# Performance work log

Measured on AMD Instinct MI355X. Metric: run time of the kernel, lower is better.

The kernel has to match this reference:

```python
import jax, jax.numpy as jnp
import numpy as np

WS = 7   # window_size
SS = 3   # shift_size = window_size // 2
NH = 16  # num_heads


def _rel_pos_index(ws):
    coords = np.stack(np.meshgrid(np.arange(ws), np.arange(ws), indexing='ij'))  # (2, ws, ws)
    cf = coords.reshape(2, -1)
    rel = (cf[:, :, None] - cf[:, None, :]).transpose(1, 2, 0)
    rel[:, :, 0] += ws - 1
    rel[:, :, 1] += ws - 1
    rel[:, :, 0] *= 2 * ws - 1
    return rel.sum(-1)  # (ws*ws, ws*ws) int

REL_IDX = _rel_pos_index(WS)


def _attn_mask(h, w, ws, ss):
    img = np.zeros((h, w))
    sls = (slice(0, -ws), slice(-ws, -ss), slice(-ss, None))
    cnt = 0
    for i in sls:
        for j in sls:
            img[i, j] = cnt
            cnt += 1
    mw = img.reshape(h // ws, ws, w // ws, ws).transpose(0, 2, 1, 3).reshape(-1, ws * ws)
    d = mw[:, None, :] - mw[:, :, None]  # (nW, N, N)
    return np.where(d != 0, -100.0, 0.0).astype(np.float32)


def _part(x, ws):
    b, h, w, c = x.shape
    return x.reshape(b, h // ws, ws, w // ws, ws, c).transpose(0, 1, 3, 2, 4, 5).reshape(-1, ws * ws, c)


def _rev(win, ws, h, w):
    c = win.shape[-1]
    b = win.shape[0] // ((h // ws) * (w // ws))
    return win.reshape(b, h // ws, w // ws, ws, ws, c).transpose(0, 1, 3, 2, 4, 5).reshape(b, h, w, c)


def _ln(x, g, b):
    m = x.mean(-1, keepdims=True)
    v = x.var(-1, keepdims=True)
    return (x - m) / jnp.sqrt(v + 1e-5) * g + b


def _wattn(x, qkv_w, qkv_b, proj_w, proj_b, table, mask):
    B_, N, C = x.shape
    hd = C // NH
    scale = hd ** -0.5
    qkv = (x @ qkv_w.T + qkv_b).reshape(B_, N, 3, NH, hd).transpose(2, 0, 3, 1, 4)
    q, k, v = qkv[0] * scale, qkv[1], qkv[2]  # (B_, NH, N, hd)
    attn = jnp.einsum('bhnd,bhmd->bhnm', q, k)
    bias = table[REL_IDX.reshape(-1)].reshape(N, N, NH).transpose(2, 0, 1)  # (NH, N, N)
    attn = attn + bias[None]
    if mask is not None:
        nW = mask.shape[0]
        attn = (attn.reshape(B_ // nW, nW, NH, N, N) + mask[None, :, None]).reshape(B_, NH, N, N)
    attn = jax.nn.softmax(attn, axis=-1)
    out = jnp.einsum('bhnm,bhmd->bhnd', attn, v).transpose(0, 2, 1, 3).reshape(B_, N, C)
    return out @ proj_w.T + proj_b


def _mlp(x, w1, b1, w2, b2):
    return jax.nn.gelu(x @ w1.T + b1, approximate=False) @ w2.T + b2


def _forward(x, w_norm1_g, w_norm1_b, w_qkv_w, w_qkv_b, w_proj_w, w_proj_b, w_table,
             w_norm2_g, w_norm2_b, w_fc1_w, w_fc1_b, w_fc2_w, w_fc2_b,
             sw_norm1_g, sw_norm1_b, sw_qkv_w, sw_qkv_b, sw_proj_w, sw_proj_b, sw_table,
             sw_norm2_g, sw_norm2_b, sw_fc1_w, sw_fc1_b, sw_fc2_w, sw_fc2_b):
    b, c, h, w = x.shape
    x = jnp.transpose(x, (0, 2, 3, 1)).reshape(b, h * w, c)  # (B, HW, C)
    shortcut = x
    xn = _ln(x, w_norm1_g, w_norm1_b).reshape(b, h, w, c)
    aw = _wattn(_part(xn, WS), w_qkv_w, w_qkv_b, w_proj_w, w_proj_b, w_table, None)
    x = shortcut + _rev(aw, WS, h, w).reshape(b, h * w, c)
    x = x + _mlp(_ln(x, w_norm2_g, w_norm2_b), w_fc1_w, w_fc1_b, w_fc2_w, w_fc2_b)
    # shifted-window branch (shift_size > 0 since min(h,w) > window_size)
    xn = _ln(x, sw_norm1_g, sw_norm1_b)
    mask = jnp.asarray(_attn_mask(h, w, WS, SS))
    shifted = jnp.roll(xn.reshape(b, h, w, c), (-SS, -SS), axis=(1, 2))
    sa = _wattn(_part(shifted, WS), sw_qkv_w, sw_qkv_b, sw_proj_w, sw_proj_b, sw_table, mask)
    shifted = jnp.roll(_rev(sa, WS, h, w), (SS, SS), axis=(1, 2)).reshape(b, h * w, c)
    # NOTE: source adds the residual to the *normalized* activations here; kept faithful.
    x = xn + shifted
    x = x + _mlp(_ln(x, sw_norm2_g, sw_norm2_b), sw_fc1_w, sw_fc1_b, sw_fc2_w, sw_fc2_b)
    return x.reshape(b, h, w, c)


def setup_inputs() -> dict:
    key = jax.random.key(0)
    ks = jax.random.split(key, 32)
    B, C, H, W = 8, 512, 56, 56
    Cm = 4 * C
    T = (2 * WS - 1) ** 2

    def rn(k, shape, s=0.02):
        return jax.random.normal(k, shape, jnp.float32) * s

    d = {'x': jax.random.normal(ks[0], (B, C, H, W), jnp.float32)}
    for i, p in enumerate(['w', 'sw']):
        o = 1 + i * 6
        d[p + '_norm1_g'] = jnp.ones((C,), jnp.float32)
        d[p + '_norm1_b'] = jnp.zeros((C,), jnp.float32)
        d[p + '_qkv_w'] = rn(ks[o], (3 * C, C))
        d[p + '_qkv_b'] = jnp.zeros((3 * C,), jnp.float32)
        d[p + '_proj_w'] = rn(ks[o + 1], (C, C))
        d[p + '_proj_b'] = jnp.zeros((C,), jnp.float32)
        d[p + '_table'] = rn(ks[o + 2], (T, NH))
        d[p + '_norm2_g'] = jnp.ones((C,), jnp.float32)
        d[p + '_norm2_b'] = jnp.zeros((C,), jnp.float32)
        d[p + '_fc1_w'] = rn(ks[o + 3], (Cm, C))
        d[p + '_fc1_b'] = jnp.zeros((Cm,), jnp.float32)
        d[p + '_fc2_w'] = rn(ks[o + 4], (C, Cm))
        d[p + '_fc2_b'] = jnp.zeros((C,), jnp.float32)
    return d


def reference(x, w_norm1_g, w_norm1_b, w_qkv_w, w_qkv_b, w_proj_w, w_proj_b, w_table,
              w_norm2_g, w_norm2_b, w_fc1_w, w_fc1_b, w_fc2_w, w_fc2_b,
              sw_norm1_g, sw_norm1_b, sw_qkv_w, sw_qkv_b, sw_proj_w, sw_proj_b, sw_table,
              sw_norm2_g, sw_norm2_b, sw_fc1_w, sw_fc1_b, sw_fc2_w, sw_fc2_b):
    return _forward(x, w_norm1_g, w_norm1_b, w_qkv_w, w_qkv_b, w_proj_w, w_proj_b, w_table,
                    w_norm2_g, w_norm2_b, w_fc1_w, w_fc1_b, w_fc2_w, w_fc2_b,
                    sw_norm1_g, sw_norm1_b, sw_qkv_w, sw_qkv_b, sw_proj_w, sw_proj_b, sw_table,
                    sw_norm2_g, sw_norm2_b, sw_fc1_w, sw_fc1_b, sw_fc2_w, sw_fc2_b)
```

## Files before the change

kernel.cpp:

```cpp
#include <hip/hip_runtime.h>
#include <hip/hip_bf16.h>

using bf16 = __hip_bfloat16;

#define B_      8
#define C_      512
#define H_      56
#define W_      56
#define HW_     3136
#define M_      25088
#define NH_     16
#define HD_     32
#define WS_     7
#define NT_     49

typedef __attribute__((ext_vector_type(8))) short bf16x8;
typedef __attribute__((ext_vector_type(4))) float f32x4;

#define AS1(p) ((const __attribute__((address_space(1))) void*)(p))
#define AS3(p) ((__attribute__((address_space(3))) void*)(p))

__device__ inline float bf2f(const bf16 v) {
    unsigned short u = *reinterpret_cast<const unsigned short*>(&v);
    return __uint_as_float((unsigned)u << 16);
}
__device__ inline unsigned short f2bfu(float f) {
    bf16 h = __float2bfloat16(f);
    return *reinterpret_cast<unsigned short*>(&h);
}
__device__ inline float rdv(const float* p) { return *p; }
__device__ inline float rdv(const bf16* p)  { return bf2f(*p); }
__device__ inline void stv(float* p, float v) { *p = v; }
__device__ inline void stv(bf16* p, float v)  { *p = __float2bfloat16(v); }

__device__ inline float gelu_t(float v) {
    const float u = v * (0.79788456080286536f + 0.035677408136300125f * v * v);
    const float e = __expf(2.0f * u);
    return 0.5f * v * (2.0f - 2.0f / (e + 1.0f));
}

__global__ void k_detect(const void* g1, int* flag) {
    const unsigned short* u = (const unsigned short*)g1;
    *flag = (u[0] == 0x3F80u) ? 1 : 0;
}

struct WArgs {
    const void* src[26];
    bf16*       dst[26];
    int         n[26];
};
__global__ __launch_bounds__(256) void k_convert_all(WArgs a, const int* flag) {
    const int isb = *flag;
    const int gid = blockIdx.x * 256 + threadIdx.x;
    const int stride = gridDim.x * 256;
    #pragma unroll 1
    for (int w = 0; w < 26; ++w) {
        const int n = a.n[w];
        bf16* d = a.dst[w];
        if (isb) {
            const unsigned short* s = (const unsigned short*)a.src[w];
            for (int i = gid; i < n; i += stride) ((unsigned short*)d)[i] = s[i];
        } else {
            const float* s = (const float*)a.src[w];
            for (int i = gid; i < n; i += stride) d[i] = __float2bfloat16(s[i]);
        }
    }
}

__global__ __launch_bounds__(256) void k_transpose_in(const void* xin, bf16* X,
                                                      const int* flag) {
    __shared__ float tile[32][33];
    const int isb = *flag;
    const int p0 = blockIdx.x * 32, c0 = blockIdx.y * 32, b = blockIdx.z;
    const int tp = threadIdx.x & 31, tc = threadIdx.x >> 5;
    const size_t ibase = (size_t)b * C_ * HW_;
    #pragma unroll
    for (int i = 0; i < 4; ++i) {
        const int c = tc + i * 8;
        const size_t idx = ibase + (size_t)(c0 + c) * HW_ + p0 + tp;
        tile[c][tp] = isb ? bf2f(((const bf16*)xin)[idx]) : ((const float*)xin)[idx];
    }
    __syncthreads();
    const int wc = threadIdx.x & 31, wp = threadIdx.x >> 5;
    bf16* dst = X + (size_t)b * HW_ * C_;
    #pragma unroll
    for (int i = 0; i < 4; ++i) {
        const int p = wp + i * 8;
        dst[(size_t)(p0 + p) * C_ + c0 + wc] = __float2bfloat16(tile[wc][p]);
    }
}

__global__ __launch_bounds__(128) void k_layernorm(const bf16* __restrict__ X,
                                                   const bf16* __restrict__ g,
                                                   const bf16* __restrict__ bta,
                                                   bf16* __restrict__ XN) {
    const int tok = blockIdx.x;
    const ushort4 u = reinterpret_cast<const ushort4*>(X + (size_t)tok * C_)[threadIdx.x];
    float4 v;
    v.x = __uint_as_float((unsigned)u.x << 16);
    v.y = __uint_as_float((unsigned)u.y << 16);
    v.z = __uint_as_float((unsigned)u.z << 16);
    v.w = __uint_as_float((unsigned)u.w << 16);
    float s  = v.x + v.y + v.z + v.w;
    float s2 = v.x * v.x + v.y * v.y + v.z * v.z + v.w * v.w;
    #pragma unroll
    for (int o = 32; o > 0; o >>= 1) { s += __shfl_down(s, o); s2 += __shfl_down(s2, o); }
    __shared__ float sh[4];
    if ((threadIdx.x & 63) == 0) { sh[threadIdx.x >> 6] = s; sh[2 + (threadIdx.x >> 6)] = s2; }
    __syncthreads();
    const float ts = sh[0] + sh[1], ts2 = sh[2] + sh[3];
    const float m = ts * (1.0f / C_);
    const float var = ts2 * (1.0f / C_) - m * m;
    const float r = rsqrtf(var + 1e-5f);
    const int c = threadIdx.x * 4;
    ushort4 o;
    o.x = f2bfu((v.x - m) * r * bf2f(g[c + 0]) + bf2f(bta[c + 0]));
    o.y = f2bfu((v.y - m) * r * bf2f(g[c + 1]) + bf2f(bta[c + 1]));
    o.z = f2bfu((v.z - m) * r * bf2f(g[c + 2]) + bf2f(bta[c + 2]));
    o.w = f2bfu((v.w - m) * r * bf2f(g[c + 3]) + bf2f(bta[c + 3]));
    reinterpret_cast<ushort4*>(XN + (size_t)tok * C_)[threadIdx.x] = o;
}

template <typename TADD, typename TO, bool GELU, bool ADD, bool FINAL>
__global__ __launch_bounds__(512, 2) void k_gemm8(const bf16* __restrict__ A,
                                                  const bf16* __restrict__ Wt,
                                                  const bf16* __restrict__ bias,
                                                  const TADD* __restrict__ addp,
                                                  TO* __restrict__ out,
                                                  const int* flag,
                                                  int N, int K) {
    __shared__ bf16 sA[2][2][128 * 64];
    __shared__ bf16 sB[2][2][128 * 64];
    const int tid  = threadIdx.x;
    const int lane = tid & 63;
    const int wid  = tid >> 6;
    const int wr   = wid >> 2;
    const int wc2  = wid & 3;
    const int bh   = wc2 >> 1;
    const int brl  = (wc2 & 1) * 64;

    const int nwg  = gridDim.x;
    const int orig = blockIdx.x;
    const int nx = nwg >> 3, rr_ = nwg & 7;
    const int xcd = orig & 7, offw = orig >> 3;
    const int wg = (xcd < rr_ ? xcd * (nx + 1) : rr_ * (nx + 1) + (xcd - rr_) * nx) + offw;
    const int gx = N >> 8;
    const int m0 = (wg / gx) * 256, n0 = (wg % gx) * 256;

    const f32x4 vz = {0.f, 0.f, 0.f, 0.f};
    f32x4 acc[8][4];
    #pragma unroll
    for (int i = 0; i < 8; ++i)
        #pragma unroll
        for (int j = 0; j < 4; ++j) acc[i][j] = vz;

    const int sr8  = lane >> 3;
    const int schk = (lane & 7) ^ sr8;
    const bf16* gA0 = A  + (size_t)(m0 + sr8) * K + schk * 8;
    const bf16* gB0 = Wt + (size_t)(n0 + sr8) * K + schk * 8;

    const int l15 = lane & 15, g4 = lane >> 4;
    const int NTL = K >> 6;
    const int NITER = NTL >> 1;

    auto stageA = [&](int d, int h, int T) {
        const int kt = T << 6;
        #pragma unroll
        for (int p = 0; p < 2; ++p) {
            const int q = wid * 2 + p;
            __builtin_amdgcn_global_load_lds(
                AS1(gA0 + (size_t)(h * 128 + q * 8) * K + kt),
                AS3(&sA[d][h][q * 512]), 16, 0, 0);
        }
    };
    auto stageB = [&](int d, int h, int T) {
        const int kt = T << 6;
        #pragma unroll
        for (int p = 0; p < 2; ++p) {
            const int q = wid * 2 + p;
            __builtin_amdgcn_global_load_lds(
                AS1(gB0 + (size_t)(h * 128 + q * 8) * K + kt),
                AS3(&sB[d][h][q * 512]), 16, 0, 0);
        }
    };

    stageA(0, 0, 0); stageA(0, 1, 0);
    stageB(0, 0, 0); stageB(0, 1, 0);
    stageB(1, 0, 1); stageB(1, 1, 1);
    asm volatile("s_waitcnt vmcnt(4)" ::: "memory");
    __builtin_amdgcn_s_barrier();

    #pragma unroll 1
    for (int it = 0; it < NITER; ++it) {
        const bool nl = (it < NITER - 1);
        #pragma unroll
        for (int half = 0; half < 2; ++half) {
            bf16x8 bfr[4][2];
            #pragma unroll
            for (int q = 0; q < 4; ++q) {
                if (q == 0) {
                    #pragma unroll
                    for (int ks = 0; ks < 2; ++ks) {
                        const int ch = ((ks << 2) | g4) ^ (l15 & 7);
                        #pragma unroll
                        for (int j = 0; j < 4; ++j) {
                            const int r = brl + j * 16 + l15;
                            bfr[j][ks] = *reinterpret_cast<const bf16x8*>(&sB[half][bh][r * 64 + ch * 8]);
                        }
                    }
                }
                bf16x8 af[2][2];
                #pragma unroll
                for (int ks = 0; ks < 2; ++ks) {
                    const int ch = ((ks << 2) | g4) ^ (l15 & 7);
                    #pragma unroll
                    for (int ii = 0; ii < 2; ++ii) {
                        const int r = (q * 2 + ii) * 16 + l15;
                        af[ii][ks] = *reinterpret_cast<const bf16x8*>(&sA[half][wr][r * 64 + ch * 8]);
                    }
                }
                if (half == 0) {
                    if (q == 0)            { stageA(1, 0, 2 * it + 1); stageA(1, 1, 2 * it + 1); }
                    else if (q == 1 && nl) { stageB(0, 0, 2 * it + 2); }
                    else if (q == 2 && nl) { stageB(0, 1, 2 * it + 2); }
                } else {
                    if (q == 0 && nl)      { stageA(0, 0, 2 * it + 2); }
                    else if (q == 1 && nl) { stageA(0, 1, 2 * it + 2); }
                    else if (q == 2 && nl) { stageB(1, 0, 2 * it + 3); }
                    else if (q == 3 && nl) { stageB(1, 1, 2 * it + 3); }
                }
                __builtin_amdgcn_s_barrier();
                asm volatile("s_waitcnt lgkmcnt(0)" ::: "memory");
                __builtin_amdgcn_s_setprio(1);
                #pragma unroll
                for (int ks = 0; ks < 2; ++ks)
                    #pragma unroll
                    for (int ii = 0; ii < 2; ++ii)
                        #pragma unroll
                        for (int j = 0; j < 4; ++j)
                            acc[q * 2 + ii][j] = __builtin_amdgcn_mfma_f32_16x16x32_bf16(
                                af[ii][ks], bfr[j][ks], acc[q * 2 + ii][j], 0, 0, 0);
                __builtin_amdgcn_s_setprio(0);
                if (q == 3) {
                    if (half == 0) {
                        if (nl) asm volatile("s_waitcnt vmcnt(4)" ::: "memory");
                        else    asm volatile("s_waitcnt vmcnt(0)" ::: "memory");
                    } else if (nl) {
                        asm volatile("s_waitcnt vmcnt(4)" ::: "memory");
                    }
                }
                __builtin_amdgcn_s_barrier();
            }
        }
    }

    int obf = 0;
    if constexpr (FINAL) obf = *flag;
    const int colBase = n0 + wc2 * 64 + l15;
    const int rowTop  = m0 + wr * 128 + g4 * 4;
    float bc[4];
    #pragma unroll
    for (int j = 0; j < 4; ++j) bc[j] = bf2f(bias[colBase + j * 16]);
    #pragma unroll
    for (int i = 0; i < 8; ++i) {
        #pragma unroll
        for (int r = 0; r < 4; ++r) {
            const int row = rowTop + i * 16 + r;
            #pragma unroll
            for (int j = 0; j < 4; ++j) {
                const int col = colBase + j * 16;
                float v = acc[i][j][r] + bc[j];
                if constexpr (GELU) v = gelu_t(v);
                if constexpr (ADD)  v += rdv(&addp[(size_t)row * N + col]);
                if constexpr (FINAL) {
                    if (obf) ((bf16*)(void*)out)[(size_t)row * N + col] = __float2bfloat16(v);
                    else     ((float*)(void*)out)[(size_t)row * N + col] = v;
                } else {
                    stv(&out[(size_t)row * N + col], v);
                }
            }
        }
    }
}

template <typename TADD, typename TO, bool GELU, bool ADD, bool FINAL>
__global__ __launch_bounds__(512, 2) void k_gemm_mfma(const bf16* __restrict__ A,
                                                      const bf16* __restrict__ Wt,
                                                      const bf16* __restrict__ bias,
                                                      const TADD* __restrict__ addp,
                                                      TO* __restrict__ out,
                                                      const int* flag,
                                                      int N, int K) {
    __shared__ bf16 sA[3][256 * 64];
    __shared__ bf16 sB[3][128 * 64];
    const int tid  = threadIdx.x;
    const int lane = tid & 63;
    const int wid  = tid >> 6;
    const int wr   = wid >> 1;
    const int wc2  = wid & 1;

    const int nwg  = gridDim.x;
    const int orig = blockIdx.x;
    const int nx = nwg >> 3, rr_ = nwg & 7;
    const int xcd = orig & 7, offw = orig >> 3;
    const int wg = (xcd < rr_ ? xcd * (nx + 1) : rr_ * (nx + 1) + (xcd - rr_) * nx) + offw;
    const int gx = N >> 7;
    const int m0 = (wg / gx) * 256, n0 = (wg % gx) * 128;

    const f32x4 vz = {0.f, 0.f, 0.f, 0.f};
    f32x4 acc[4][4];
    #pragma unroll
    for (int i = 0; i < 4; ++i)
        #pragma unroll
        for (int j = 0; j < 4; ++j) acc[i][j] = vz;

    const int sr8  = lane >> 3;
    const int schk = (lane & 7) ^ sr8;
    const bf16* gA0 = A  + (size_t)(m0 + sr8) * K + schk * 8;
    const bf16* gB0 = Wt + (size_t)(n0 + sr8) * K + schk * 8;

    const int l15 = lane & 15, g4 = lane >> 4;
    const int NTLE = K >> 6;

    #pragma unroll
    for (int tt = 0; tt < 3; ++tt) {
        const int kt = tt << 6;
        #pragma unroll
        for (int p = 0; p < 4; ++p) {
            const int q = wid * 4 + p;
            __builtin_amdgcn_global_load_lds(AS1(gA0 + (size_t)(q * 8) * K + kt),
                                             AS3(&sA[tt][q * 512]), 16, 0, 0);
        }
        #pragma unroll
        for (int p = 0; p < 2; ++p) {
            const int q = wid * 2 + p;
            __builtin_amdgcn_global_load_lds(AS1(gB0 + (size_t)(q * 8) * K + kt),
                                             AS3(&sB[tt][q * 512]), 16, 0, 0);
        }
    }

    for (int t = 0; t < NTLE; ++t) {
        const int rem = NTLE - 1 - t;
        if (rem >= 2)      asm volatile("s_waitcnt vmcnt(12)" ::: "memory");
        else if (rem == 1) asm volatile("s_waitcnt vmcnt(6)"  ::: "memory");
        else               asm volatile("s_waitcnt vmcnt(0)"  ::: "memory");
        __builtin_amdgcn_s_barrier();

        const int buf = t % 3;
        bf16x8 bfr[4][2];
        #pragma unroll
        for (int ks = 0; ks < 2; ++ks) {
            const int ch = ((ks << 2) | g4) ^ (l15 & 7);
            #pragma unroll
            for (int j = 0; j < 4; ++j) {
                const int rowB = wc2 * 64 + j * 16 + l15;
                bfr[j][ks] = *reinterpret_cast<const bf16x8*>(&sB[buf][rowB * 64 + ch * 8]);
            }
        }
        const int ch0 = g4 ^ (l15 & 7);
        const int ch1 = (4 | g4) ^ (l15 & 7);
        __builtin_amdgcn_s_setprio(1);
        #pragma unroll
        for (int i = 0; i < 4; ++i) {
            const int rowA = wr * 64 + i * 16 + l15;
            const bf16x8 a0 = *reinterpret_cast<const bf16x8*>(&sA[buf][rowA * 64 + ch0 * 8]);
            const bf16x8 a1 = *reinterpret_cast<const bf16x8*>(&sA[buf][rowA * 64 + ch1 * 8]);
            #pragma unroll
            for (int j = 0; j < 4; ++j) {
                acc[i][j] = __builtin_amdgcn_mfma_f32_16x16x32_bf16(a0, bfr[j][0], acc[i][j], 0, 0, 0);
                acc[i][j] = __builtin_amdgcn_mfma_f32_16x16x32_bf16(a1, bfr[j][1], acc[i][j], 0, 0, 0);
            }
        }
        __builtin_amdgcn_s_setprio(0);

        asm volatile("s_waitcnt lgkmcnt(0)" ::: "memory");
        __builtin_amdgcn_s_barrier();

        const int tn = t + 3;
        if (tn < NTLE) {
            const int kt = tn << 6;
            #pragma unroll
            for (int p = 0; p < 4; ++p) {
                const int q = wid * 4 + p;
                __builtin_amdgcn_global_load_lds(AS1(gA0 + (size_t)(q * 8) * K + kt),
                                                 AS3(&sA[buf][q * 512]), 16, 0, 0);
            }
            #pragma unroll
            for (int p = 0; p < 2; ++p) {
                const int q = wid * 2 + p;
                __builtin_amdgcn_global_load_lds(AS1(gB0 + (size_t)(q * 8) * K + kt),
                                                 AS3(&sB[buf][q * 512]), 16, 0, 0);
            }
        }
    }

    int obf = 0;
    if constexpr (FINAL) obf = *flag;
    const int colBase = n0 + wc2 * 64 + l15;
    const int rowTop  = m0 + wr * 64 + g4 * 4;
    float bc[4];
    #pragma unroll
    for (int j = 0; j < 4; ++j) bc[j] = bf2f(bias[colBase + j * 16]);
    #pragma unroll
    for (int i = 0; i < 4; ++i) {
        #pragma unroll
        for (int r = 0; r < 4; ++r) {
            const int row = rowTop + i * 16 + r;
            #pragma unroll
            for (int j = 0; j < 4; ++j) {
                const int col = colBase + j * 16;
                float v = acc[i][j][r] + bc[j];
                if constexpr (GELU) v = gelu_t(v);
                if constexpr (ADD)  v += rdv(&addp[(size_t)row * N + col]);
                if constexpr (FINAL) {
                    if (obf) ((bf16*)(void*)out)[(size_t)row * N + col] = __float2bfloat16(v);
                    else     ((float*)(void*)out)[(size_t)row * N + col] = v;
                } else {
                    stv(&out[(size_t)row * N + col], v);
                }
            }
        }
    }
}

__global__ __launch_bounds__(256) void k_mktbl(const bf16* __restrict__ table,
                                               bf16* __restrict__ out, int shifted) {
    const int bh = blockIdx.x;
    const int cls = bh >> 4, h = bh & 15;
    const int rowE = shifted ? (cls >> 1) : 0;
    const int colE = shifted ? (cls & 1) : 0;
    for (int e = threadIdx.x; e < 64 * 64; e += 256) {
        const int i = e >> 6, j = e & 63;
        float v;
        if (i < NT_ && j < NT_) {
            const int yi = i / WS_, xi = i % WS_, yj = j / WS_, xj = j % WS_;
            const int ridx = (yi - yj + 6) * 13 + (xi - xj + 6);
            v = bf2f(table[ridx * NH_ + h]);
            const int ri = (rowE ? (yi < 4 ? 1 : 2) : 0) * 3 + (colE ? (xi < 4 ? 1 : 2) : 0);
            const int rj = (rowE ? (yj < 4 ? 1 : 2) : 0) * 3 + (colE ? (xj < 4 ? 1 : 2) : 0);
            if (ri != rj) v -= 100.f;
        } else if (j >= NT_) {
            v = -3e30f;
        } else {
            v = 0.f;
        }
        out[((size_t)bh << 12) + e] = __float2bfloat16(v);
    }
}

template <int SS, bool SHIFTED>
__global__ __launch_bounds__(64) void k_attn_mfma(const bf16* __restrict__ QKV,
                                                  const bf16* __restrict__ tbl,
                                                  bf16* __restrict__ O) {
    __shared__ __align__(16) short uQK[5120];
    __shared__ __align__(16) short uVt[2304];
    __shared__ int toks[NT_];
    short* Qs = uQK;
    short* Ks = uQK + 2560;
    short* Ps = uQK;

    const int lane = threadIdx.x;
    const int head = blockIdx.x & 15;
    const int win  = blockIdx.x >> 4;
    const int bl = win >> 6, w64 = win & 63;
    const int wy = w64 >> 3, wx = w64 & 7;

    if (lane < NT_) {
        const int dy = lane / WS_, dx = lane % WS_;
        const int sr = wy * WS_ + dy, scn = wx * WS_ + dx;
        const int r = (sr + SS) % H_, c = (scn + SS) % W_;
        toks[lane] = bl * HW_ + r * W_ + c;
    }
    __syncthreads();

    const int g4 = lane >> 4, l15 = lane & 15;
    const int tsg = lane >> 2, csg = (lane & 3) * 8;

    #pragma unroll
    for (int rr = 0; rr < 4; ++rr) {
        const int t = rr * 16 + tsg;
        bf16x8 qv = {0,0,0,0,0,0,0,0}, kv = {0,0,0,0,0,0,0,0}, vv = {0,0,0,0,0,0,0,0};
        if (t < NT_) {
            const bf16* base = QKV + (size_t)toks[t] * 1536 + head * HD_ + csg;
            qv = *reinterpret_cast<const bf16x8*>(base);
            kv = *reinterpret_cast<const bf16x8*>(base + 512);
            vv = *reinterpret_cast<const bf16x8*>(base + 1024);
        }
        *reinterpret_cast<bf16x8*>(&Qs[t * 40 + csg]) = qv;
        *reinterpret_cast<bf16x8*>(&Ks[t * 40 + csg]) = kv;
        #pragma unroll
        for (int e = 0; e < 8; ++e) uVt[(csg + e) * 72 + t] = ((const short*)&vv)[e];
    }
    __syncthreads();

    bf16x8 aq[4], bk[4];
    #pragma unroll
    for (int f = 0; f < 4; ++f) {
        aq[f] = *reinterpret_cast<const bf16x8*>(&Qs[(f * 16 + l15) * 40 + g4 * 8]);
        bk[f] = *reinterpret_cast<const bf16x8*>(&Ks[(f * 16 + l15) * 40 + g4 * 8]);
    }
    const f32x4 vz = {0.f, 0.f, 0.f, 0.f};
    f32x4 sacc[4][4];
    #pragma unroll
    for (int qi = 0; qi < 4; ++qi)
        #pragma unroll
        for (int kj = 0; kj < 4; ++kj)
            sacc[qi][kj] = __builtin_amdgcn_mfma_f32_16x16x32_bf16(aq[qi], bk[kj], vz, 0, 0, 0);
    __syncthreads();

    const int cls = SHIFTED ? (((wy == 7) ? 2 : 0) + ((wx == 7) ? 1 : 0)) : 0;
    const bf16* tb = tbl + (((size_t)(cls * NH_ + head)) << 12);
    const float scale = 0.17677669529663687f;
    #pragma unroll
    for (int qi = 0; qi < 4; ++qi) {
        #pragma unroll
        for (int r = 0; r < 4; ++r) {
            const int i = qi * 16 + g4 * 4 + r;
            const bf16* trow = tb + (i << 6);
            float sv[4];
            #pragma unroll
            for (int kj = 0; kj < 4; ++kj)
                sv[kj] = sacc[qi][kj][r] * scale + bf2f(trow[kj * 16 + l15]);
            float mx = fmaxf(fmaxf(sv[0], sv[1]), fmaxf(sv[2], sv[3]));
            #pragma unroll
            for (int d = 1; d <= 8; d <<= 1) mx = fmaxf(mx, __shfl_xor(mx, d));
            float p[4], sum = 0.f;
            #pragma unroll
            for (int kj = 0; kj < 4; ++kj) { p[kj] = __expf(sv[kj] - mx); sum += p[kj]; }
            #pragma unroll
            for (int d = 1; d <= 8; d <<= 1) sum += __shfl_xor(sum, d);
            const float inv = 1.0f / sum;
            #pragma unroll
            for (int kj = 0; kj < 4; ++kj)
                Ps[i * 72 + kj * 16 + l15] = (short)f2bfu(p[kj] * inv);
        }
    }
    __syncthreads();

    f32x4 oacc[4][2];
    #pragma unroll
    for (int qi = 0; qi < 4; ++qi) { oacc[qi][0] = vz; oacc[qi][1] = vz; }
    #pragma unroll
    for (int ks = 0; ks < 2; ++ks) {
        bf16x8 bv[2];
        #pragma unroll
        for (int dj = 0; dj < 2; ++dj)
            bv[dj] = *reinterpret_cast<const bf16x8*>(&uVt[(dj * 16 + l15) * 72 + ks * 32 + g4 * 8]);
        #pragma unroll
        for (int qi = 0; qi < 4; ++qi) {
            const bf16x8 ap = *reinterpret_cast<const bf16x8*>(&Ps[(qi * 16 + l15) * 72 + ks * 32 + g4 * 8]);
            #pragma unroll
            for (int dj = 0; dj < 2; ++dj)
                oacc[qi][dj] = __builtin_amdgcn_mfma_f32_16x16x32_bf16(ap, bv[dj], oacc[qi][dj], 0, 0, 0);
        }
    }
    #pragma unroll
    for (int qi = 0; qi < 4; ++qi) {
        #pragma unroll
        for (int r = 0; r < 4; ++r) {
            const int i = qi * 16 + g4 * 4 + r;
            if (i < NT_) {
                const size_t ob = (size_t)toks[i] * C_ + head * HD_ + l15;
                O[ob]      = __float2bfloat16(oacc[qi][0][r]);
                O[ob + 16] = __float2bfloat16(oacc[qi][1][r]);
            }
        }
    }
}

extern "C" void kernel_launch(void* const* d_in, const int* in_sizes, int n_in,
                              void* d_out, int out_size, void* d_ws, size_t ws_size,
                              hipStream_t stream) {
    (void)out_size; (void)ws_size;
    char* ws = (char*)d_ws;
    const size_t WEIGHT_RESERVE = 12651520;
    bf16*  WC   = (bf16*)ws;
    int*   FLG  = (int*)(ws + WEIGHT_RESERVE);
    bf16*  TBL1 = (bf16*)(ws + WEIGHT_RESERVE + 1024);
    bf16*  TBL2 = (bf16*)(ws + WEIGHT_RESERVE + 1024 + 131072);
    bf16*  X    = (bf16*)(ws + WEIGHT_RESERVE + 656384);
    bf16*  XN   = X + (size_t)M_ * C_;
    char*  BIG  = (char*)(XN + (size_t)M_ * C_);

    size_t offs[27];
    size_t off = 0;
    for (int i = 1; i < n_in && i < 27; ++i) { offs[i] = off; off += (size_t)((in_sizes[i] + 7) & ~7); }
    auto wc = [&](int i) { return (const bf16*)(WC + offs[i]); };

    k_detect<<<1, 1, 0, stream>>>(d_in[1], FLG);
    {
        WArgs a;
        for (int i = 1; i < 27; ++i) {
            a.src[i - 1] = d_in[i];
            a.dst[i - 1] = WC + offs[i];
            a.n[i - 1]   = in_sizes[i];
        }
        k_convert_all<<<512, 256, 0, stream>>>(a, FLG);
    }
    k_mktbl<<<16, 256, 0, stream>>>(wc(7),  TBL1, 0);
    k_mktbl<<<64, 256, 0, stream>>>(wc(20), TBL2, 1);

    const dim3 gT(HW_ / 32, C_ / 32, B_);
    k_transpose_in<<<gT, 256, 0, stream>>>(d_in[0], X, FLG);

    bf16* QKV = (bf16*)BIG;
    bf16* ATT = (bf16*)(BIG + (size_t)M_ * 1536 * 2);
    bf16* HID = (bf16*)BIG;

    const int gQ = (1536 / 256) * (M_ / 256);
    const int gF = (2048 / 256) * (M_ / 256);
    const int gP = (512 / 128)  * (M_ / 256);
    const int gO = (512 / 256)  * (M_ / 256);
    const dim3 gA(B_ * 64 * NH_);

    k_layernorm<<<M_, 128, 0, stream>>>(X, wc(1), wc(2), XN);
    k_gemm8<bf16, bf16, false, false, false><<<gQ, 512, 0, stream>>>(
        XN, wc(3), wc(4), (const bf16*)nullptr, QKV, nullptr, 1536, C_);
    k_attn_mfma<0, false><<<gA, 64, 0, stream>>>(QKV, TBL1, ATT);
    k_gemm_mfma<bf16, bf16, false, true, false><<<gP, 512, 0, stream>>>(
        ATT, wc(5), wc(6), X, X, nullptr, C_, C_);
    k_layernorm<<<M_, 128, 0, stream>>>(X, wc(8), wc(9), XN);
    k_gemm8<bf16, bf16, true, false, false><<<gF, 512, 0, stream>>>(
        XN, wc(10), wc(11), (const bf16*)nullptr, HID, nullptr, 2048, C_);
    k_gemm8<bf16, bf16, false, true, false><<<gO, 512, 0, stream>>>(
        HID, wc(12), wc(13), X, X, nullptr, C_, 2048);
    k_layernorm<<<M_, 128, 0, stream>>>(X, wc(14), wc(15), XN);
    k_gemm8<bf16, bf16, false, false, false><<<gQ, 512, 0, stream>>>(
        XN, wc(16), wc(17), (const bf16*)nullptr, QKV, nullptr, 1536, C_);
    k_attn_mfma<3, true><<<gA, 64, 0, stream>>>(QKV, TBL2, ATT);
    k_gemm_mfma<bf16, bf16, false, true, false><<<gP, 512, 0, stream>>>(
        ATT, wc(18), wc(19), XN, X, nullptr, C_, C_);
    k_layernorm<<<M_, 128, 0, stream>>>(X, wc(21), wc(22), XN);
    k_gemm8<bf16, bf16, true, false, false><<<gF, 512, 0, stream>>>(
        XN, wc(23), wc(24), (const bf16*)nullptr, HID, nullptr, 2048, C_);
    k_gemm8<bf16, float, false, true, true><<<gO, 512, 0, stream>>>(
        HID, wc(25), wc(26), X, (float*)d_out, FLG, C_, 2048);
}
```

Measured before the change: 794.6 us.

## Fuse residual add and LayerNorm into full-row output-projection GEMM

Replaces the proj and fc2 GEMMs with a new kernel where each block computes a full 128x512 output row tile. The bias and residual are added and the row LayerNorm statistics are reduced in registers and LDS, so the kernel writes both X and the normalized XN. This removes three separate layernorm launches and the extra read and write of X they need. In exchange the GEMM uses a smaller K-tile (32) with only double buffering and a full vmcnt(0) wait each step, which can reduce latency hiding. The grid is also smaller (196 blocks), so occupancy may drop. There is a possible aliasing hazard when XN is both the residual input and the output in the shifted block, since different blocks touch different rows.

```diff
diff --git a/kernel.cpp b/kernel.cpp
--- a/kernel.cpp
+++ b/kernel.cpp
@@ -283,140 +283,170 @@
     }
 }
 
-template <typename TADD, typename TO, bool GELU, bool ADD, bool FINAL>
-__global__ __launch_bounds__(512, 2) void k_gemm_mfma(const bf16* __restrict__ A,
-                                                      const bf16* __restrict__ Wt,
-                                                      const bf16* __restrict__ bias,
-                                                      const TADD* __restrict__ addp,
-                                                      TO* __restrict__ out,
-                                                      const int* flag,
-                                                      int N, int K) {
-    __shared__ bf16 sA[3][256 * 64];
-    __shared__ bf16 sB[3][128 * 64];
+template <typename TADD, bool LN, bool FINAL>
+__global__ __launch_bounds__(512, 2) void k_gemm_ln(const bf16* __restrict__ A,
+                                                    const bf16* __restrict__ Wt,
+                                                    const bf16* __restrict__ bias,
+                                                    const TADD* __restrict__ addp,
+                                                    const bf16* __restrict__ lng,
+                                                    const bf16* __restrict__ lnb,
+                                                    bf16* __restrict__ Xout,
+                                                    bf16* __restrict__ XNout,
+                                                    void* fout, const int* flag,
+                                                    int K) {
+    __shared__ bf16 sA[2][128 * 32];
+    __shared__ bf16 sB[2][512 * 32];
     const int tid  = threadIdx.x;
     const int lane = tid & 63;
     const int wid  = tid >> 6;
-    const int wr   = wid >> 1;
-    const int wc2  = wid & 1;
+    const int wr   = wid >> 2;
+    const int wc2  = wid & 3;
 
     const int nwg  = gridDim.x;
     const int orig = blockIdx.x;
     const int nx = nwg >> 3, rr_ = nwg & 7;
     const int xcd = orig & 7, offw = orig >> 3;
     const int wg = (xcd < rr_ ? xcd * (nx + 1) : rr_ * (nx + 1) + (xcd - rr_) * nx) + offw;
-    const int gx = N >> 7;
-    const int m0 = (wg / gx) * 256, n0 = (wg % gx) * 128;
+    const int m0 = wg * 128;
 
     const f32x4 vz = {0.f, 0.f, 0.f, 0.f};
-    f32x4 acc[4][4];
+    f32x4 acc[4][8];
     #pragma unroll
     for (int i = 0; i < 4; ++i)
         #pragma unroll
-        for (int j = 0; j < 4; ++j) acc[i][j] = vz;
-
-    const int sr8  = lane >> 3;
-    const int schk = (lane & 7) ^ sr8;
-    const bf16* gA0 = A  + (size_t)(m0 + sr8) * K + schk * 8;
-    const bf16* gB0 = Wt + (size_t)(n0 + sr8) * K + schk * 8;
+        for (int j = 0; j < 8; ++j) acc[i][j] = vz;
+
+    const int sr16 = lane >> 2;
+    const int schk = (lane & 3) ^ ((lane >> 3) & 3);
+    const bf16* gA0 = A  + (size_t)(m0 + sr16) * K + schk * 8;
+    const bf16* gB0 = Wt + (size_t)sr16 * K + schk * 8;
 
     const int l15 = lane & 15, g4 = lane >> 4;
-    const int NTLE = K >> 6;
-
-    #pragma unroll
-    for (int tt = 0; tt < 3; ++tt) {
-        const int kt = tt << 6;
+    const int NT32 = K >> 5;
+
+    auto stage = [&](int T, int d) {
+        const int kt = T << 5;
+        {
+            const int q = wid;
+            __builtin_amdgcn_global_load_lds(AS1(gA0 + (size_t)(q * 16) * K + kt),
+                                             AS3(&sA[d][q * 512]), 16, 0, 0);
+        }
         #pragma unroll
         for (int p = 0; p < 4; ++p) {
             const int q = wid * 4 + p;
-            __builtin_amdgcn_global_load_lds(AS1(gA0 + (size_t)(q * 8) * K + kt),
-                                             AS3(&sA[tt][q * 512]), 16, 0, 0);
-        }
-        #pragma unroll
-        for (int p = 0; p < 2; ++p) {
-            const int q = wid * 2 + p;
-            __builtin_amdgcn_global_load_lds(AS1(gB0 + (size_t)(q * 8) * K + kt),
-                                             AS3(&sB[tt][q * 512]), 16, 0, 0);
-        }
-    }
-
-    for (int t = 0; t < NTLE; ++t) {
-        const int rem = NTLE - 1 - t;
-        if (rem >= 2)      asm volatile("s_waitcnt vmcnt(12)" ::: "memory");
-        else if (rem == 1) asm volatile("s_waitcnt vmcnt(6)"  ::: "memory");
-        else               asm volatile("s_waitcnt vmcnt(0)"  ::: "memory");
+            __builtin_amdgcn_global_load_lds(AS1(gB0 + (size_t)(q * 16) * K + kt),
+                                             AS3(&sB[d][q * 512]), 16, 0, 0);
+        }
+    };
+
+    int cur = 0;
+    stage(0, 0);
+
+    for (int t = 0; t < NT32; ++t) {
+        asm volatile("s_waitcnt vmcnt(0)" ::: "memory");
         __builtin_amdgcn_s_barrier();
 
-        const int buf = t % 3;
-        bf16x8 bfr[4][2];
-        #pragma unroll
-        for (int ks = 0; ks < 2; ++ks) {
-            const int ch = ((ks << 2) | g4) ^ (l15 & 7);
-            #pragma unroll
-            for (int j = 0; j < 4; ++j) {
-                const int rowB = wc2 * 64 + j * 16 + l15;
-                bfr[j][ks] = *reinterpret_cast<const bf16x8*>(&sB[buf][rowB * 64 + ch * 8]);
-            }
-        }
-        const int ch0 = g4 ^ (l15 & 7);
-        const int ch1 = (4 | g4) ^ (l15 & 7);
-        __builtin_amdgcn_s_setprio(1);
+        if (t + 1 < NT32) stage(t + 1, cur ^ 1);
+
+        const int ch = g4 ^ ((l15 >> 1) & 3);
+        bf16x8 bfr[8];
+        #pragma unroll
+        for (int j = 0; j < 8; ++j) {
+            const int rowB = wc2 * 128 + j * 16 + l15;
+            bfr[j] = *reinterpret_cast<const bf16x8*>(&sB[cur][rowB * 32 + ch * 8]);
+        }
+        bf16x8 af[4];
         #pragma unroll
         for (int i = 0; i < 4; ++i) {
             const int rowA = wr * 64 + i * 16 + l15;
-            const bf16x8 a0 = *reinterpret_cast<const bf16x8*>(&sA[buf][rowA * 64 + ch0 * 8]);
-            const bf16x8 a1 = *reinterpret_cast<const bf16x8*>(&sA[buf][rowA * 64 + ch1 * 8]);
-            #pragma unroll
-            for (int j = 0; j < 4; ++j) {
-                acc[i][j] = __builtin_amdgcn_mfma_f32_16x16x32_bf16(a0, bfr[j][0], acc[i][j], 0, 0, 0);
-                acc[i][j] = __builtin_amdgcn_mfma_f32_16x16x32_bf16(a1, bfr[j][1], acc[i][j], 0, 0, 0);
-            }
-        }
+            af[i] = *reinterpret_cast<const bf16x8*>(&sA[cur][rowA * 32 + ch * 8]);
+        }
+
+        __builtin_amdgcn_s_setprio(1);
+        #pragma unroll
+        for (int i = 0; i < 4; ++i)
+            #pragma unroll
+            for (int j = 0; j < 8; ++j)
+                acc[i][j] = __builtin_amdgcn_mfma_f32_16x16x32_bf16(af[i], bfr[j], acc[i][j], 0, 0, 0);
         __builtin_amdgcn_s_setprio(0);
 
         asm volatile("s_waitcnt lgkmcnt(0)" ::: "memory");
         __builtin_amdgcn_s_barrier();
-
-        const int tn = t + 3;
-        if (tn < NTLE) {
-            const int kt = tn << 6;
-            #pragma unroll
-            for (int p = 0; p < 4; ++p) {
-                const int q = wid * 4 + p;
-                __builtin_amdgcn_global_load_lds(AS1(gA0 + (size_t)(q * 8) * K + kt),
-                                                 AS3(&sA[buf][q * 512]), 16, 0, 0);
+        cur ^= 1;
+    }
+
+    const int colBase = wc2 * 128 + l15;
+    float bc[8];
+    #pragma unroll
+    for (int j = 0; j < 8; ++j) bc[j] = bf2f(bias[colBase + j * 16]);
+
+    if constexpr (FINAL) {
+        const int obf = *flag;
+        #pragma unroll
+        for (int i = 0; i < 4; ++i) {
+            #pragma unroll
+            for (int r = 0; r < 4; ++r) {
+                const int row = m0 + wr * 64 + i * 16 + g4 * 4 + r;
+                #pragma unroll
+                for (int j = 0; j < 8; ++j) {
+                    const int col = colBase + j * 16;
+                    float v = acc[i][j][r] + bc[j] + rdv(&addp[(size_t)row * 512 + col]);
+                    if (obf) ((bf16*)fout)[(size_t)row * 512 + col] = __float2bfloat16(v);
+                    else     ((float*)fout)[(size_t)row * 512 + col] = v;
+                }
             }
-            #pragma unroll
-            for (int p = 0; p < 2; ++p) {
-                const int q = wid * 2 + p;
-                __builtin_amdgcn_global_load_lds(AS1(gB0 + (size_t)(q * 8) * K + kt),
-                                                 AS3(&sB[buf][q * 512]), 16, 0, 0);
+        }
+    } else {
+        float2* scratch = (float2*)(void*)sA;
+        #pragma unroll
+        for (int i = 0; i < 4; ++i) {
+            #pragma unroll
+            for (int r = 0; r < 4; ++r) {
+                const int row = m0 + wr * 64 + i * 16 + g4 * 4 + r;
+                float s = 0.f, s2 = 0.f;
+                #pragma unroll
+                for (int j = 0; j < 8; ++j) {
+                    const int col = colBase + j * 16;
+                    float v = acc[i][j][r] + bc[j] + rdv(&addp[(size_t)row * 512 + col]);
+                    acc[i][j][r] = v;
+                    s += v; s2 += v * v;
+                }
+                #pragma unroll
+                for (int d = 1; d <= 8; d <<= 1) { s += __shfl_xor(s, d); s2 += __shfl_xor(s2, d); }
+                if (l15 == 0) {
+                    const int rl = wr * 64 + i * 16 + g4 * 4 + r;
+                    scratch[rl * 4 + wc2] = make_float2(s, s2);
+                }
             }
         }
-    }
-
-    int obf = 0;
-    if constexpr (FINAL) obf = *flag;
-    const int colBase = n0 + wc2 * 64 + l15;
-    const int rowTop  = m0 + wr * 64 + g4 * 4;
-    float bc[4];
-    #pragma unroll
-    for (int j = 0; j < 4; ++j) bc[j] = bf2f(bias[colBase + j * 16]);
-    #pragma unroll
-    for (int i = 0; i < 4; ++i) {
-        #pragma unroll
-        for (int r = 0; r < 4; ++r) {
-            const int row = rowTop + i * 16 + r;
-            #pragma unroll
-            for (int j = 0; j < 4; ++j) {
-                const int col = colBase + j * 16;
-                float v = acc[i][j][r] + bc[j];
-                if constexpr (GELU) v = gelu_t(v);
-                if constexpr (ADD)  v += rdv(&addp[(size_t)row * N + col]);
-                if constexpr (FINAL) {
-                    if (obf) ((bf16*)(void*)out)[(size_t)row * N + col] = __float2bfloat16(v);
-                    else     ((float*)(void*)out)[(size_t)row * N + col] = v;
-                } else {
-                    stv(&out[(size_t)row * N + col], v);
+        __syncthreads();
+        float gj[8], bj[8];
+        #pragma unroll
+        for (int j = 0; j < 8; ++j) {
+            gj[j] = bf2f(lng[colBase + j * 16]);
+            bj[j] = bf2f(lnb[colBase + j * 16]);
+        }
+        #pragma unroll
+        for (int i = 0; i < 4; ++i) {
+            #pragma unroll
+            for (int r = 0; r < 4; ++r) {
+                const int rl = wr * 64 + i * 16 + g4 * 4 + r;
+                float ts = 0.f, ts2 = 0.f;
+                #pragma unroll
+                for (int w = 0; w < 4; ++w) {
+                    const float2 p = scratch[rl * 4 + w];
+                    ts += p.x; ts2 += p.y;
+                }
+                const float m  = ts * (1.0f / 512.0f);
+                const float va = ts2 * (1.0f / 512.0f) - m * m;
+                const float rs = rsqrtf(va + 1e-5f);
+                const size_t row = (size_t)(m0 + rl);
+                #pragma unroll
+                for (int j = 0; j < 8; ++j) {
+                    const int col = colBase + j * 16;
+                    const float v = acc[i][j][r];
+                    Xout [row * 512 + col] = __float2bfloat16(v);
+                    XNout[row * 512 + col] = __float2bfloat16((v - m) * rs * gj[j] + bj[j]);
                 }
             }
         }
@@ -609,30 +639,26 @@
 
     const int gQ = (1536 / 256) * (M_ / 256);
     const int gF = (2048 / 256) * (M_ / 256);
-    const int gP = (512 / 128)  * (M_ / 256);
-    const int gO = (512 / 256)  * (M_ / 256);
+    const int gL = M_ / 128;
     const dim3 gA(B_ * 64 * NH_);
 
     k_layernorm<<<M_, 128, 0, stream>>>(X, wc(1), wc(2), XN);
     k_gemm8<bf16, bf16, false, false, false><<<gQ, 512, 0, stream>>>(
         XN, wc(3), wc(4), (const bf16*)nullptr, QKV, nullptr, 1536, C_);
     k_attn_mfma<0, false><<<gA, 64, 0, stream>>>(QKV, TBL1, ATT);
-    k_gemm_mfma<bf16, bf16, false, true, false><<<gP, 512, 0, stream>>>(
-        ATT, wc(5), wc(6), X, X, nullptr, C_, C_);
-    k_layernorm<<<M_, 128, 0, stream>>>(X, wc(8), wc(9), XN);
+    k_gemm_ln<bf16, true, false><<<gL, 512, 0, stream>>>(
+        ATT, wc(5), wc(6), X, wc(8), wc(9), X, XN, nullptr, nullptr, C_);
     k_gemm8<bf16, bf16, true, false, false><<<gF, 512, 0, stream>>>(
         XN, wc(10), wc(11), (const bf16*)nullptr, HID, nullptr, 2048, C_);
-    k_gemm8<bf16, bf16, false, true, false><<<gO, 512, 0, stream>>>(
-        HID, wc(12), wc(13), X, X, nullptr, C_, 2048);
-    k_layernorm<<<M_, 128, 0, stream>>>(X, wc(14), wc(15), XN);
+    k_gemm_ln<bf16, true, false><<<gL, 512, 0, stream>>>(
+        HID, wc(12), wc(13), X, wc(14), wc(15), X, XN, nullptr, nullptr, 2048);
     k_gemm8<bf16, bf16, false, false, false><<<gQ, 512, 0, stream>>>(
         XN, wc(16), wc(17), (const bf16*)nullptr, QKV, nullptr, 1536, C_);
     k_attn_mfma<3, true><<<gA, 64, 0, stream>>>(QKV, TBL2, ATT);
-    k_gemm_mfma<bf16, bf16, false, true, false><<<gP, 512, 0, stream>>>(
-        ATT, wc(18), wc(19), XN, X, nullptr, C_, C_);
-    k_layernorm<<<M_, 128, 0, stream>>>(X, wc(21), wc(22), XN);
+    k_gemm_ln<bf16, true, false><<<gL, 512, 0, stream>>>(
+        ATT, wc(18), wc(19), XN, wc(21), wc(22), X, XN, nullptr, nullptr, C_);
     k_gemm8<bf16, bf16, true, false, false><<<gF, 512, 0, stream>>>(
         XN, wc(23), wc(24), (const bf16*)nullptr, HID, nullptr, 2048, C_);
-    k_gemm8<bf16, float, false, true, true><<<gO, 512, 0, stream>>>(
-        HID, wc(25), wc(26), X, (float*)d_out, FLG, C_, 2048);
-}
+    k_gemm_ln<bf16, false, true><<<gL, 512, 0, stream>>>(
+        HID, wc(25), wc(26), X, nullptr, nullptr, nullptr, nullptr, d_out, FLG, 2048);
+}
```

Measured after the change: 852.1 us. 7.2% more time.
